# Kernel optimization log

Hardware: AMD Instinct MI355X
Metric: run time of the kernel (lower is better)

Reference implementation:

```python
import jax, jax.numpy as jnp
from jax import lax
import numpy as np

# GConv2d config (matches init_kwargs)
OUT_TRANSFORMS = 4  # rotations: 0, 90, 180, 270 degrees
STRIDE = 1
PADDING = 1


def setup_inputs() -> dict:
    key = jax.random.key(0)
    k1, k2, k3, k4 = jax.random.split(key, 4)
    B, IC_EFF, H, W = 16, 256, 64, 64   # IC_EFF = in_channels * in_transformations
    OC, K, F = 64, 4, 3                 # out_channels, num_dynamic_kernels, filter_size
    x = jax.random.normal(k1, (B, IC_EFF, H, W), dtype=jnp.float32)
    W_fc = jax.random.normal(k2, (K, IC_EFF), dtype=jnp.float32) * (1.0 / np.sqrt(IC_EFF))
    b_fc = jnp.zeros((K,), dtype=jnp.float32)
    kernel_bank = jax.random.normal(k3, (K, OC, IC_EFF, F, F), dtype=jnp.float32)
    return {"x": x, "W_fc": W_fc, "b_fc": b_fc, "kernel_bank": kernel_bank}


def reference(x, W_fc, b_fc, kernel_bank):
    B, C, H, W = x.shape
    # Dynamic routing: global average pool -> linear -> softmax over kernel bank
    pooled = x.mean(axis=(2, 3))                      # [B, C]
    coeffs = jax.nn.softmax(pooled @ W_fc.T + b_fc, axis=1)  # [B, K]
    # Sample-specific base kernels: mix of kernel bank
    base = jnp.einsum('bk,kocij->bocij', coeffs, kernel_bank)  # [B, oc, C, f, f]
    # P4 orientation expansion: rotate kernel spatially, stack along out-channels
    oriented = jnp.concatenate(
        [jnp.rot90(base, k, axes=(-2, -1)) for k in range(OUT_TRANSFORMS)], axis=1
    )  # [B, 4*oc, C, f, f]
    O, f = oriented.shape[1], oriented.shape[-1]
    # Batched per-sample conv via grouped convolution (one launch instead of B)
    xg = x.reshape(1, B * C, H, W)
    kg = oriented.reshape(B * O, C, f, f)
    out = lax.conv_general_dilated(
        xg, kg,
        window_strides=(STRIDE, STRIDE),
        padding=[(PADDING, PADDING), (PADDING, PADDING)],
        dimension_numbers=('NCHW', 'OIHW', 'NCHW'),
        feature_group_count=B,
    )  # [1, B*O, H', W']
    Ho, Wo = out.shape[-2], out.shape[-1]
    return out.reshape(B, O, Ho, Wo)
```

## Files before the change

### kernel.cpp

```cpp
#include <hip/hip_runtime.h>

#define B_  16
#define C_  256
#define O_  256

typedef short    bf16x8 __attribute__((ext_vector_type(8)));
typedef float    f32x16 __attribute__((ext_vector_type(16)));
typedef unsigned u32x4  __attribute__((ext_vector_type(4)));
typedef unsigned u32x2  __attribute__((ext_vector_type(2)));

#define XROW_SH  1056
#define XBC_SH   (66 * XROW_SH)
#define XT_BYTES ((size_t)B_ * 16 * XBC_SH * 2)

#define WTILE_SH 9216
#define WORP_BYTES ((size_t)B_ * 16 * 4 * WTILE_SH * 2)

#define XBUF_SH  10752

__device__ __forceinline__ unsigned cvtpk(float lo, float hi) {
    unsigned r;
    asm("v_cvt_pk_bf16_f32 %0, %1, %2" : "=v"(r) : "v"(lo), "v"(hi));
    return r;
}

__device__ __forceinline__ void gload16(const void* g, void* l) {
    __builtin_amdgcn_global_load_lds(
        (const __attribute__((address_space(1))) unsigned int*)g,
        (__attribute__((address_space(3))) unsigned int*)l, 16, 0, 0);
}

__global__ __launch_bounds__(256) void xprep_kernel(const float* __restrict__ x,
                                                    short* __restrict__ xT,
                                                    float* __restrict__ pooled4) {
    const int cc = blockIdx.x;
    const int b  = blockIdx.y;
    const int z  = blockIdx.z;
    const int t  = threadIdx.x;

    __shared__ float xsf[2][16][67];

    short* xTb = xT + (size_t)(b * 16 + cc) * XBC_SH;
    const float* xb = x + ((size_t)(b * C_ + cc * 16) << 12);

    {
        u32x4 zv = {0, 0, 0, 0};
        int nz = 64 + ((z == 0 || z == 3) ? 132 : 0);
        for (int i = t; i < nz; i += 256) {
            int off;
            if (i < 64) {
                int row = z * 16 + 1 + (i >> 2);
                int sub = i & 3;
                off = row * XROW_SH + (sub >> 1) * 528 + ((sub & 1) ? 65 * 8 : 0);
            } else {
                off = (z == 0 ? 0 : 65 * XROW_SH) + (i - 64) * 8;
            }
            *(u32x4*)&xTb[off] = zv;
        }
    }

    const int cl = t >> 4;
    const int xq = t & 15;
    float s = 0.f;

    for (int it = 0; it < 8; ++it) {
        const int ybase = z * 16 + it * 2;
        const float* src = xb + ((size_t)cl << 12) + ybase * 64 + xq * 4;
        float4 v0 = *(const float4*)src;
        float4 v1 = *(const float4*)(src + 64);
        s += v0.x + v0.y + v0.z + v0.w + v1.x + v1.y + v1.z + v1.w;
        __syncthreads();
        float* d0 = &xsf[0][cl][xq * 4];
        d0[0] = v0.x; d0[1] = v0.y; d0[2] = v0.z; d0[3] = v0.w;
        float* d1 = &xsf[1][cl][xq * 4];
        d1[0] = v1.x; d1[1] = v1.y; d1[2] = v1.z; d1[3] = v1.w;
        __syncthreads();
        const int yy  = t >> 7;
        const int lhh = (t >> 6) & 1;
        const int col = (t & 63) + 1;
        const float* rr = &xsf[yy][lhh * 8][col - 1];
        u32x4 d;
        d[0] = cvtpk(rr[0 * 67], rr[1 * 67]);
        d[1] = cvtpk(rr[2 * 67], rr[3 * 67]);
        d[2] = cvtpk(rr[4 * 67], rr[5 * 67]);
        d[3] = cvtpk(rr[6 * 67], rr[7 * 67]);
        *(u32x4*)&xTb[(ybase + yy + 1) * XROW_SH + lhh * 528 + col * 8] = d;
    }

#pragma unroll
    for (int off = 1; off < 16; off <<= 1) s += __shfl_xor(s, off, 64);
    if (xq == 0)
        pooled4[(z * B_ + b) * C_ + cc * 16 + cl] = s * (1.0f / 4096.0f);
}

__global__ __launch_bounds__(256) void mix_kernel(const float* __restrict__ bank,
                                                  const float* __restrict__ pooled4,
                                                  const float* __restrict__ W_fc,
                                                  const float* __restrict__ b_fc,
                                                  short* __restrict__ worp) {
    const int b  = blockIdx.x;
    const int cc = blockIdx.y;
    const int t  = threadIdx.x, lane = t & 63, wid = t >> 6;

    __shared__ float bankL[4 * 64 * 37];
    __shared__ float lg[4];

    {
        float s = 0.f;
#pragma unroll
        for (int q = 0; q < 4; ++q) {
            int c = lane * 4 + q;
            float pv = pooled4[b * C_ + c] + pooled4[(B_ + b) * C_ + c]
                     + pooled4[(2 * B_ + b) * C_ + c] + pooled4[(3 * B_ + b) * C_ + c];
            s += pv * W_fc[wid * C_ + c];
        }
#pragma unroll
        for (int off = 32; off; off >>= 1) s += __shfl_down(s, off, 64);
        if (lane == 0) lg[wid] = s + b_fc[wid];
    }
    __syncthreads();
    float l0 = lg[0], l1 = lg[1], l2 = lg[2], l3 = lg[3];
    float mx = fmaxf(fmaxf(l0, l1), fmaxf(l2, l3));
    float e0 = expf(l0 - mx), e1 = expf(l1 - mx), e2 = expf(l2 - mx), e3 = expf(l3 - mx);
    float inv = 1.f / (e0 + e1 + e2 + e3);
    const float cf0 = e0 * inv, cf1 = e1 * inv, cf2 = e2 * inv, cf3 = e3 * inv;

    const int oq  = t >> 6;
    const int o64 = t & 63;

    for (int sub = 0; sub < 4; ++sub) {
        __syncthreads();
        for (int i = t; i < 9216; i += 256) {
            int run = i / 36, e = i % 36;
            bankL[run * 37 + e] = bank[((size_t)run * C_ + cc * 16 + sub * 4) * 9 + e];
        }
        __syncthreads();

        const int lhs = sub >> 1;
        const float* bp = &bankL[o64 * 37];
#pragma unroll
        for (int ti = 0; ti < 3; ++ti)
#pragma unroll
            for (int tj = 0; tj < 3; ++tj) {
                int si, sj;
                if      (oq == 0) { si = ti;     sj = tj;     }
                else if (oq == 1) { si = tj;     sj = 2 - ti; }
                else if (oq == 2) { si = 2 - ti; sj = 2 - tj; }
                else              { si = 2 - tj; sj = ti;     }
                const int sij = si * 3 + sj;
                float v[4];
#pragma unroll
                for (int c4 = 0; c4 < 4; ++c4) {
                    const float* q = bp + c4 * 9 + sij;
                    v[c4] = cf0 * q[0] + cf1 * q[64 * 37] + cf2 * q[2 * 64 * 37]
                          + cf3 * q[3 * 64 * 37];
                }
                u32x2 d = { cvtpk(v[0], v[1]), cvtpk(v[2], v[3]) };
                size_t base = (((((size_t)(b * 16 + cc) * 4 + oq) * 9 + (ti * 3 + tj)) * 2
                                + lhs) * 64 + o64) * 8 + (sub & 1) * 4;
                *(u32x2*)&worp[base] = d;
            }
    }
}

__global__ __launch_bounds__(256, 2)
void conv_mfma(const short* __restrict__ xT, const short* __restrict__ worp,
               float* __restrict__ out) {
    __shared__ short lds[2 * XBUF_SH + 2 * WTILE_SH];

    const int g    = blockIdx.x;
    const int w    = (g & 7) * 64 + (g >> 3);
    const int oq   = w & 3;
    const int m    = w >> 2;
    const int rowt = m & 7;
    const int b    = m >> 3;
    const int y0   = rowt * 8;

    const int t    = threadIdx.x;
    const int lane = t & 63;
    const int wid  = t >> 6;
    const int l31  = lane & 31;
    const int lh   = lane >> 5;

    const char* xsrcB = (const char*)xT
        + ((size_t)(b * 16) * XBC_SH + (size_t)y0 * XROW_SH) * 2 + lane * 16;
    const char* wsrcB = (const char*)worp
        + (((size_t)(b * 16) * 4) + oq) * (WTILE_SH * 2) + lane * 16;

#define STAGE(ccc, p)                                                           \
    { const char* xs = xsrcB + (size_t)(ccc) * (XBC_SH * 2);                    \
      const char* ws = wsrcB + (size_t)(ccc) * (4 * WTILE_SH * 2);              \
      char* xd = (char*)lds + (p) * (XBUF_SH * 2);                              \
      char* wd = (char*)lds + 2 * (XBUF_SH * 2) + (p) * (WTILE_SH * 2);         \
      for (int u = wid; u < 21; u += 4) gload16(xs + u * 1024, xd + u * 1024);  \
      for (int u = wid; u < 18; u += 4) gload16(ws + u * 1024, wd + u * 1024); }

    f32x16 acc0[4] = {}, acc1[4] = {};

    STAGE(0, 0);
    __syncthreads();

    for (int cc = 0; cc < 16; ++cc) {
        const int p = cc & 1;
        if (cc < 15) STAGE(cc + 1, p ^ 1);
        const short* xcur = lds + p * XBUF_SH;
        const short* wcur = lds + 2 * XBUF_SH + p * WTILE_SH;
        __builtin_amdgcn_s_setprio(1);
#pragma unroll
        for (int i = 0; i < 3; ++i)
#pragma unroll
            for (int j = 0; j < 3; ++j) {
                const int tap = i * 3 + j;
                const short* wp = wcur + ((tap * 2 + lh) * 64 + l31) * 8;
                bf16x8 A0 = *(const bf16x8*)wp;
                bf16x8 A1 = *(const bf16x8*)(wp + 256);
#pragma unroll
                for (int pf = 0; pf < 4; ++pf) {
                    const int rl   = 2 * wid + (pf >> 1) + i;
                    const int colb = (pf & 1) * 32 + j;
                    bf16x8 Bv = *(const bf16x8*)
                        &xcur[((rl * 2 + lh) * 66 + colb + l31) * 8];
                    acc0[pf] = __builtin_amdgcn_mfma_f32_32x32x16_bf16(A0, Bv, acc0[pf], 0, 0, 0);
                    acc1[pf] = __builtin_amdgcn_mfma_f32_32x32x16_bf16(A1, Bv, acc1[pf], 0, 0, 0);
                }
            }
        __builtin_amdgcn_s_setprio(0);
        __syncthreads();
    }
#undef STAGE

#pragma unroll
    for (int pf = 0; pf < 4; ++pf) {
        const int yb  = y0 + 2 * wid + (pf >> 1);
        const int xcb = 32 * (pf & 1) + l31;
#pragma unroll
        for (int r = 0; r < 16; ++r) {
            const int orow = (r & 3) + 8 * (r >> 2) + 4 * lh;
            const int o0   = oq * 64 + orow;
            out[((size_t)(b * O_ + o0)      << 12) + yb * 64 + xcb] = acc0[pf][r];
            out[((size_t)(b * O_ + o0 + 32) << 12) + yb * 64 + xcb] = acc1[pf][r];
        }
    }
}

extern "C" void kernel_launch(void* const* d_in, const int* in_sizes, int n_in,
                              void* d_out, int out_size, void* d_ws, size_t ws_size,
                              hipStream_t stream) {
    const float* x    = (const float*)d_in[0];
    const float* W_fc = (const float*)d_in[1];
    const float* b_fc = (const float*)d_in[2];
    const float* bank = (const float*)d_in[3];
    float* out = (float*)d_out;

    short* xTb     = (short*)d_ws;
    short* worp    = (short*)((char*)d_ws + XT_BYTES);
    float* pooled4 = (float*)((char*)d_ws + XT_BYTES + WORP_BYTES);

    xprep_kernel<<<dim3(16, 16, 4), 256, 0, stream>>>(x, xTb, pooled4);
    mix_kernel<<<dim3(B_, 16), 256, 0, stream>>>(bank, pooled4, W_fc, b_fc, worp);
    conv_mfma<<<512, 256, 0, stream>>>(xTb, worp, out);
}
```

Before: 112.7 us.

## Reuse input row fragments across taps, double-buffer xprep LDS, nontemporal stores

The conv main loop now loads each input row's six bf16 B-fragments into registers once and reuses them across the three vertical taps, rotating two register row buffers. Before, every tap reloaded its fragments from LDS. This cuts LDS reads per k-chunk from 36 to 24 per wave, at the cost of higher VGPR pressure. Separately, the xprep kernel double-buffers its shared staging array to drop one barrier per iteration, and output stores become nontemporal so the large fp32 output does not pollute the cache.

```diff
diff --git a/kernel.cpp b/kernel.cpp
--- a/kernel.cpp
+++ b/kernel.cpp
@@ -38,7 +38,7 @@
     const int z  = blockIdx.z;
     const int t  = threadIdx.x;
 
-    __shared__ float xsf[2][16][67];
+    __shared__ float xsf[2][2][16][67];
 
     short* xTb = xT + (size_t)(b * 16 + cc) * XBC_SH;
     const float* xb = x + ((size_t)(b * C_ + cc * 16) << 12);
@@ -61,24 +61,24 @@
 
     const int cl = t >> 4;
     const int xq = t & 15;
+    const int yy  = t >> 7;
+    const int lhh = (t >> 6) & 1;
+    const int col = (t & 63) + 1;
     float s = 0.f;
 
     for (int it = 0; it < 8; ++it) {
+        const int bufi  = it & 1;
         const int ybase = z * 16 + it * 2;
         const float* src = xb + ((size_t)cl << 12) + ybase * 64 + xq * 4;
         float4 v0 = *(const float4*)src;
         float4 v1 = *(const float4*)(src + 64);
         s += v0.x + v0.y + v0.z + v0.w + v1.x + v1.y + v1.z + v1.w;
-        __syncthreads();
-        float* d0 = &xsf[0][cl][xq * 4];
+        float* d0 = &xsf[bufi][0][cl][xq * 4];
         d0[0] = v0.x; d0[1] = v0.y; d0[2] = v0.z; d0[3] = v0.w;
-        float* d1 = &xsf[1][cl][xq * 4];
+        float* d1 = &xsf[bufi][1][cl][xq * 4];
         d1[0] = v1.x; d1[1] = v1.y; d1[2] = v1.z; d1[3] = v1.w;
         __syncthreads();
-        const int yy  = t >> 7;
-        const int lhh = (t >> 6) & 1;
-        const int col = (t & 63) + 1;
-        const float* rr = &xsf[yy][lhh * 8][col - 1];
+        const float* rr = &xsf[bufi][yy][lhh * 8][col - 1];
         u32x4 d;
         d[0] = cvtpk(rr[0 * 67], rr[1 * 67]);
         d[1] = cvtpk(rr[2 * 67], rr[3 * 67]);
@@ -195,6 +195,28 @@
       for (int u = wid; u < 21; u += 4) gload16(xs + u * 1024, xd + u * 1024);  \
       for (int u = wid; u < 18; u += 4) gload16(ws + u * 1024, wd + u * 1024); }
 
+#define BRD(r, s) (*(const bf16x8*)&xcur[(((r) * 2 + lh) * 66 + (s) + l31) * 8])
+#define LOADROW(R, r)                                                           \
+    { R[0] = BRD(r, 0);  R[1] = BRD(r, 1);  R[2] = BRD(r, 2);                   \
+      R[3] = BRD(r, 32); R[4] = BRD(r, 33); R[5] = BRD(r, 34); }
+
+#define TAPROW(i, RA, RB)                                                       \
+    _Pragma("unroll")                                                           \
+    for (int j = 0; j < 3; ++j) {                                               \
+        const int tap = (i) * 3 + j;                                            \
+        const short* wp = wcur + ((tap * 2 + lh) * 64 + l31) * 8;               \
+        bf16x8 A0 = *(const bf16x8*)wp;                                         \
+        bf16x8 A1 = *(const bf16x8*)(wp + 256);                                 \
+        acc0[0] = __builtin_amdgcn_mfma_f32_32x32x16_bf16(A0, RA[j],     acc0[0], 0, 0, 0); \
+        acc1[0] = __builtin_amdgcn_mfma_f32_32x32x16_bf16(A1, RA[j],     acc1[0], 0, 0, 0); \
+        acc0[1] = __builtin_amdgcn_mfma_f32_32x32x16_bf16(A0, RA[3 + j], acc0[1], 0, 0, 0); \
+        acc1[1] = __builtin_amdgcn_mfma_f32_32x32x16_bf16(A1, RA[3 + j], acc1[1], 0, 0, 0); \
+        acc0[2] = __builtin_amdgcn_mfma_f32_32x32x16_bf16(A0, RB[j],     acc0[2], 0, 0, 0); \
+        acc1[2] = __builtin_amdgcn_mfma_f32_32x32x16_bf16(A1, RB[j],     acc1[2], 0, 0, 0); \
+        acc0[3] = __builtin_amdgcn_mfma_f32_32x32x16_bf16(A0, RB[3 + j], acc0[3], 0, 0, 0); \
+        acc1[3] = __builtin_amdgcn_mfma_f32_32x32x16_bf16(A1, RB[3 + j], acc1[3], 0, 0, 0); \
+    }
+
     f32x16 acc0[4] = {}, acc1[4] = {};
 
     STAGE(0, 0);
@@ -205,29 +227,23 @@
         if (cc < 15) STAGE(cc + 1, p ^ 1);
         const short* xcur = lds + p * XBUF_SH;
         const short* wcur = lds + 2 * XBUF_SH + p * WTILE_SH;
+
+        bf16x8 R0[6], R1[6];
         __builtin_amdgcn_s_setprio(1);
-#pragma unroll
-        for (int i = 0; i < 3; ++i)
-#pragma unroll
-            for (int j = 0; j < 3; ++j) {
-                const int tap = i * 3 + j;
-                const short* wp = wcur + ((tap * 2 + lh) * 64 + l31) * 8;
-                bf16x8 A0 = *(const bf16x8*)wp;
-                bf16x8 A1 = *(const bf16x8*)(wp + 256);
-#pragma unroll
-                for (int pf = 0; pf < 4; ++pf) {
-                    const int rl   = 2 * wid + (pf >> 1) + i;
-                    const int colb = (pf & 1) * 32 + j;
-                    bf16x8 Bv = *(const bf16x8*)
-                        &xcur[((rl * 2 + lh) * 66 + colb + l31) * 8];
-                    acc0[pf] = __builtin_amdgcn_mfma_f32_32x32x16_bf16(A0, Bv, acc0[pf], 0, 0, 0);
-                    acc1[pf] = __builtin_amdgcn_mfma_f32_32x32x16_bf16(A1, Bv, acc1[pf], 0, 0, 0);
-                }
-            }
+        LOADROW(R0, 2 * wid);
+        LOADROW(R1, 2 * wid + 1);
+        TAPROW(0, R0, R1)
+        LOADROW(R0, 2 * wid + 2)
+        TAPROW(1, R1, R0)
+        LOADROW(R1, 2 * wid + 3)
+        TAPROW(2, R0, R1)
         __builtin_amdgcn_s_setprio(0);
         __syncthreads();
     }
 #undef STAGE
+#undef BRD
+#undef LOADROW
+#undef TAPROW
 
 #pragma unroll
     for (int pf = 0; pf < 4; ++pf) {
@@ -237,8 +253,10 @@
         for (int r = 0; r < 16; ++r) {
             const int orow = (r & 3) + 8 * (r >> 2) + 4 * lh;
             const int o0   = oq * 64 + orow;
-            out[((size_t)(b * O_ + o0)      << 12) + yb * 64 + xcb] = acc0[pf][r];
-            out[((size_t)(b * O_ + o0 + 32) << 12) + yb * 64 + xcb] = acc1[pf][r];
+            __builtin_nontemporal_store(acc0[pf][r],
+                &out[((size_t)(b * O_ + o0)      << 12) + yb * 64 + xcb]);
+            __builtin_nontemporal_store(acc1[pf][r],
+                &out[((size_t)(b * O_ + o0 + 32) << 12) + yb * 64 + xcb]);
         }
     }
 }
```

After: 111.1 us. No clear change (-1.5%).

## Rework x prep without LDS, load conv weights to registers, nontemporal output stores

Applied to the files above, without the earlier changes.

The x-prep kernel now has each block handle 8 channels and converts them straight from global loads into packed bf16 stores, with no LDS transpose staging. The launch grid doubles to match. The conv kernel stops staging weights in LDS: each lane loads its 18 weight fragments from global into registers per channel chunk, which shrinks LDS use and removes those async copies. Output stores become nontemporal to avoid cache pollution. Costs are a higher register count, direct global weight-load latency inside the loop, and strided per-element reads of x in the prep kernel.

```diff
diff --git a/kernel.cpp b/kernel.cpp
--- a/kernel.cpp
+++ b/kernel.cpp
@@ -33,64 +33,58 @@
 __global__ __launch_bounds__(256) void xprep_kernel(const float* __restrict__ x,
                                                     short* __restrict__ xT,
                                                     float* __restrict__ pooled4) {
-    const int cc = blockIdx.x;
+    const int cg = blockIdx.x;
     const int b  = blockIdx.y;
     const int z  = blockIdx.z;
     const int t  = threadIdx.x;
-
-    __shared__ float xsf[2][16][67];
+    const int lane = t & 63, wv = t >> 6;
+    const int cc = cg >> 1, lh = cg & 1;
 
     short* xTb = xT + (size_t)(b * 16 + cc) * XBC_SH;
-    const float* xb = x + ((size_t)(b * C_ + cc * 16) << 12);
+    const float* xb = x + ((size_t)(b * C_ + cg * 8) << 12);
 
     {
         u32x4 zv = {0, 0, 0, 0};
-        int nz = 64 + ((z == 0 || z == 3) ? 132 : 0);
-        for (int i = t; i < nz; i += 256) {
-            int off;
-            if (i < 64) {
-                int row = z * 16 + 1 + (i >> 2);
-                int sub = i & 3;
-                off = row * XROW_SH + (sub >> 1) * 528 + ((sub & 1) ? 65 * 8 : 0);
-            } else {
-                off = (z == 0 ? 0 : 65 * XROW_SH) + (i - 64) * 8;
-            }
-            *(u32x4*)&xTb[off] = zv;
-        }
-    }
-
-    const int cl = t >> 4;
-    const int xq = t & 15;
-    float s = 0.f;
-
-    for (int it = 0; it < 8; ++it) {
-        const int ybase = z * 16 + it * 2;
-        const float* src = xb + ((size_t)cl << 12) + ybase * 64 + xq * 4;
-        float4 v0 = *(const float4*)src;
-        float4 v1 = *(const float4*)(src + 64);
-        s += v0.x + v0.y + v0.z + v0.w + v1.x + v1.y + v1.z + v1.w;
-        __syncthreads();
-        float* d0 = &xsf[0][cl][xq * 4];
-        d0[0] = v0.x; d0[1] = v0.y; d0[2] = v0.z; d0[3] = v0.w;
-        float* d1 = &xsf[1][cl][xq * 4];
-        d1[0] = v1.x; d1[1] = v1.y; d1[2] = v1.z; d1[3] = v1.w;
-        __syncthreads();
-        const int yy  = t >> 7;
-        const int lhh = (t >> 6) & 1;
-        const int col = (t & 63) + 1;
-        const float* rr = &xsf[yy][lhh * 8][col - 1];
-        u32x4 d;
-        d[0] = cvtpk(rr[0 * 67], rr[1 * 67]);
-        d[1] = cvtpk(rr[2 * 67], rr[3 * 67]);
-        d[2] = cvtpk(rr[4 * 67], rr[5 * 67]);
-        d[3] = cvtpk(rr[6 * 67], rr[7 * 67]);
-        *(u32x4*)&xTb[(ybase + yy + 1) * XROW_SH + lhh * 528 + col * 8] = d;
-    }
-
-#pragma unroll
-    for (int off = 1; off < 16; off <<= 1) s += __shfl_xor(s, off, 64);
-    if (xq == 0)
-        pooled4[(z * B_ + b) * C_ + cc * 16 + cl] = s * (1.0f / 4096.0f);
+        if (t < 32) {
+            int r   = z * 16 + 1 + (t >> 1);
+            int col = (t & 1) ? 65 : 0;
+            *(u32x4*)&xTb[r * XROW_SH + lh * 528 + col * 8] = zv;
+        }
+        if (z == 0 || z == 3) {
+            int row = (z == 0) ? 0 : 65;
+            if (t < 66) *(u32x4*)&xTb[row * XROW_SH + lh * 528 + t * 8] = zv;
+        }
+    }
+
+    float s[8] = {0.f, 0.f, 0.f, 0.f, 0.f, 0.f, 0.f, 0.f};
+    const int px = lane;
+#pragma unroll
+    for (int r = 0; r < 4; ++r) {
+        const int row = z * 16 + wv * 4 + r;
+        const float* src = xb + row * 64 + px;
+        float v[8];
+#pragma unroll
+        for (int i = 0; i < 8; ++i) { v[i] = src[(size_t)i << 12]; s[i] += v[i]; }
+        u32x4 d = { cvtpk(v[0], v[1]), cvtpk(v[2], v[3]),
+                    cvtpk(v[4], v[5]), cvtpk(v[6], v[7]) };
+        *(u32x4*)&xTb[(row + 1) * XROW_SH + lh * 528 + (px + 1) * 8] = d;
+    }
+
+#pragma unroll
+    for (int i = 0; i < 8; ++i)
+#pragma unroll
+        for (int off = 32; off; off >>= 1) s[i] += __shfl_xor(s[i], off, 64);
+
+    __shared__ float pr[4][8];
+    if (lane == 0) {
+#pragma unroll
+        for (int i = 0; i < 8; ++i) pr[wv][i] = s[i];
+    }
+    __syncthreads();
+    if (t < 8) {
+        float v = pr[0][t] + pr[1][t] + pr[2][t] + pr[3][t];
+        pooled4[(z * B_ + b) * C_ + cg * 8 + t] = v * (1.0f / 4096.0f);
+    }
 }
 
 __global__ __launch_bounds__(256) void mix_kernel(const float* __restrict__ bank,
@@ -166,7 +160,7 @@
 __global__ __launch_bounds__(256, 2)
 void conv_mfma(const short* __restrict__ xT, const short* __restrict__ worp,
                float* __restrict__ out) {
-    __shared__ short lds[2 * XBUF_SH + 2 * WTILE_SH];
+    __shared__ short lds[2 * XBUF_SH];
 
     const int g    = blockIdx.x;
     const int w    = (g & 7) * 64 + (g >> 3);
@@ -184,16 +178,14 @@
 
     const char* xsrcB = (const char*)xT
         + ((size_t)(b * 16) * XBC_SH + (size_t)y0 * XROW_SH) * 2 + lane * 16;
-    const char* wsrcB = (const char*)worp
-        + (((size_t)(b * 16) * 4) + oq) * (WTILE_SH * 2) + lane * 16;
+    const short* wq = worp + (((size_t)(b * 16) * 4) + oq) * WTILE_SH;
 
 #define STAGE(ccc, p)                                                           \
     { const char* xs = xsrcB + (size_t)(ccc) * (XBC_SH * 2);                    \
-      const char* ws = wsrcB + (size_t)(ccc) * (4 * WTILE_SH * 2);              \
       char* xd = (char*)lds + (p) * (XBUF_SH * 2);                              \
-      char* wd = (char*)lds + 2 * (XBUF_SH * 2) + (p) * (WTILE_SH * 2);         \
-      for (int u = wid; u < 21; u += 4) gload16(xs + u * 1024, xd + u * 1024);  \
-      for (int u = wid; u < 18; u += 4) gload16(ws + u * 1024, wd + u * 1024); }
+      for (int u = wid; u < 21; u += 4) gload16(xs + u * 1024, xd + u * 1024); }
+
+#define BRD(r, s) (*(const bf16x8*)&xcur[(((r) * 2 + lh) * 66 + (s) + l31) * 8])
 
     f32x16 acc0[4] = {}, acc1[4] = {};
 
@@ -202,32 +194,44 @@
 
     for (int cc = 0; cc < 16; ++cc) {
         const int p = cc & 1;
+        const short* wsc = wq + (size_t)cc * (4 * WTILE_SH);
+
+        bf16x8 Af[3][3][2];
+#pragma unroll
+        for (int i = 0; i < 3; ++i)
+#pragma unroll
+            for (int j = 0; j < 3; ++j)
+#pragma unroll
+                for (int oh = 0; oh < 2; ++oh)
+                    Af[i][j][oh] = *(const bf16x8*)
+                        (wsc + (((i * 3 + j) * 2 + lh) * 64 + oh * 32 + l31) * 8);
+
         if (cc < 15) STAGE(cc + 1, p ^ 1);
+
         const short* xcur = lds + p * XBUF_SH;
-        const short* wcur = lds + 2 * XBUF_SH + p * WTILE_SH;
         __builtin_amdgcn_s_setprio(1);
 #pragma unroll
         for (int i = 0; i < 3; ++i)
 #pragma unroll
             for (int j = 0; j < 3; ++j) {
-                const int tap = i * 3 + j;
-                const short* wp = wcur + ((tap * 2 + lh) * 64 + l31) * 8;
-                bf16x8 A0 = *(const bf16x8*)wp;
-                bf16x8 A1 = *(const bf16x8*)(wp + 256);
-#pragma unroll
-                for (int pf = 0; pf < 4; ++pf) {
-                    const int rl   = 2 * wid + (pf >> 1) + i;
-                    const int colb = (pf & 1) * 32 + j;
-                    bf16x8 Bv = *(const bf16x8*)
-                        &xcur[((rl * 2 + lh) * 66 + colb + l31) * 8];
-                    acc0[pf] = __builtin_amdgcn_mfma_f32_32x32x16_bf16(A0, Bv, acc0[pf], 0, 0, 0);
-                    acc1[pf] = __builtin_amdgcn_mfma_f32_32x32x16_bf16(A1, Bv, acc1[pf], 0, 0, 0);
-                }
+                bf16x8 B00 = BRD(2 * wid + i,     j);
+                bf16x8 B01 = BRD(2 * wid + i,     32 + j);
+                bf16x8 B10 = BRD(2 * wid + i + 1, j);
+                bf16x8 B11 = BRD(2 * wid + i + 1, 32 + j);
+                acc0[0] = __builtin_amdgcn_mfma_f32_32x32x16_bf16(Af[i][j][0], B00, acc0[0], 0, 0, 0);
+                acc1[0] = __builtin_amdgcn_mfma_f32_32x32x16_bf16(Af[i][j][1], B00, acc1[0], 0, 0, 0);
+                acc0[1] = __builtin_amdgcn_mfma_f32_32x32x16_bf16(Af[i][j][0], B01, acc0[1], 0, 0, 0);
+                acc1[1] = __builtin_amdgcn_mfma_f32_32x32x16_bf16(Af[i][j][1], B01, acc1[1], 0, 0, 0);
+                acc0[2] = __builtin_amdgcn_mfma_f32_32x32x16_bf16(Af[i][j][0], B10, acc0[2], 0, 0, 0);
+                acc1[2] = __builtin_amdgcn_mfma_f32_32x32x16_bf16(Af[i][j][1], B10, acc1[2], 0, 0, 0);
+                acc0[3] = __builtin_amdgcn_mfma_f32_32x32x16_bf16(Af[i][j][0], B11, acc0[3], 0, 0, 0);
+                acc1[3] = __builtin_amdgcn_mfma_f32_32x32x16_bf16(Af[i][j][1], B11, acc1[3], 0, 0, 0);
             }
         __builtin_amdgcn_s_setprio(0);
         __syncthreads();
     }
 #undef STAGE
+#undef BRD
 
 #pragma unroll
     for (int pf = 0; pf < 4; ++pf) {
@@ -237,8 +241,10 @@
         for (int r = 0; r < 16; ++r) {
             const int orow = (r & 3) + 8 * (r >> 2) + 4 * lh;
             const int o0   = oq * 64 + orow;
-            out[((size_t)(b * O_ + o0)      << 12) + yb * 64 + xcb] = acc0[pf][r];
-            out[((size_t)(b * O_ + o0 + 32) << 12) + yb * 64 + xcb] = acc1[pf][r];
+            __builtin_nontemporal_store(acc0[pf][r],
+                &out[((size_t)(b * O_ + o0)      << 12) + yb * 64 + xcb]);
+            __builtin_nontemporal_store(acc1[pf][r],
+                &out[((size_t)(b * O_ + o0 + 32) << 12) + yb * 64 + xcb]);
         }
     }
 }
@@ -256,7 +262,7 @@
     short* worp    = (short*)((char*)d_ws + XT_BYTES);
     float* pooled4 = (float*)((char*)d_ws + XT_BYTES + WORP_BYTES);
 
-    xprep_kernel<<<dim3(16, 16, 4), 256, 0, stream>>>(x, xTb, pooled4);
+    xprep_kernel<<<dim3(32, 16, 4), 256, 0, stream>>>(x, xTb, pooled4);
     mix_kernel<<<dim3(B_, 16), 256, 0, stream>>>(bank, pooled4, W_fc, b_fc, worp);
     conv_mfma<<<512, 256, 0, stream>>>(xTb, worp, out);
 }
```

Measured after the change: 115.7 us. 2.6% more time.
